# Optimization experiments

Measured on AMD Instinct MI355X. Metric: run time of the kernel, lower is better.

## Reference

```python
import jax, jax.numpy as jnp
import numpy as np

B, S, D, H = 4096, 200, 64, 36
BN_EPS = 1e-5
DICE_EPS = 1e-3


def setup_inputs() -> dict:
    key = jax.random.key(0)
    ks = jax.random.split(key, 6)
    return {
        "history": jax.random.normal(ks[0], (B, S, D), dtype=jnp.float32),
        "candidate": jax.random.normal(ks[1], (B, D), dtype=jnp.float32),
        "W1": jax.random.normal(ks[2], (4 * D, H), dtype=jnp.float32) * 0.05,
        "b1": jax.random.normal(ks[3], (H,), dtype=jnp.float32) * 0.05,
        "gamma": jnp.ones((H,), dtype=jnp.float32),
        "beta": jnp.zeros((H,), dtype=jnp.float32),
        "alpha": jax.random.normal(ks[4], (1,), dtype=jnp.float32),
        "W2": jax.random.normal(ks[5], (H, 1), dtype=jnp.float32) * 0.05,
        "b2": jnp.zeros((1,), dtype=jnp.float32),
    }


def reference(history, candidate, W1, b1, gamma, beta, alpha, W2, b2):
    b, s, d = history.shape
    cand = jnp.broadcast_to(candidate[:, None, :], (b, s, d))
    att_in = jnp.concatenate([cand, history, cand - history, cand * history], axis=-1)
    x = att_in.reshape(b * s, 4 * d)
    # Linear
    h = x @ W1 + b1
    # BatchNorm1d (training mode: batch statistics, biased variance)
    mu = h.mean(axis=0)
    var = h.var(axis=0)
    h = (h - mu) * jax.lax.rsqrt(var + BN_EPS) * gamma + beta
    # Dice: per-row normalization over features, eps=1e-3
    avg = h.mean(axis=1, keepdims=True)
    v = jnp.sum((h - avg) ** 2, axis=1, keepdims=True) / h.shape[1]
    ps = jax.nn.sigmoid((h - avg) / jnp.sqrt(v + DICE_EPS))
    h = ps * h + (1.0 - ps) * alpha * h
    # Output linear -> attention weight per (b, s)
    w = (h @ W2 + b2).reshape(b, s)
    # Weighted sum pooling over sequence
    return jnp.einsum("bs,bsd->bd", w, history)
```

## Files before the change

### kernel.cpp

```cpp
#include <hip/hip_runtime.h>
#include <hip/hip_bf16.h>
#include <math.h>

#define BB 4096
#define SS 200
#define DD 64
#define HH 36
#define NP 48
#define NTI 13
#define NROWSF (4096.0f * 200.0f)
#define PSTRIDE 80

typedef short bf16x8 __attribute__((ext_vector_type(8)));
typedef float f32x4 __attribute__((ext_vector_type(4)));

__device__ __forceinline__ unsigned short f2bf(float f) {
    union { float f; unsigned u; } v; v.f = f;
    unsigned r = v.u + 0x7FFFu + ((v.u >> 16) & 1u);
    return (unsigned short)(r >> 16);
}
__device__ __forceinline__ unsigned f2bf2(float a, float b) {
    union { __hip_bfloat162 h; unsigned u; } v;
    v.h = __float22bfloat162_rn(float2{a, b});
    return v.u;
}

__device__ __forceinline__ void gl_lds16(const void* g, void* l) {
    __builtin_amdgcn_global_load_lds(
        (const __attribute__((address_space(1))) unsigned*)g,
        (__attribute__((address_space(3))) unsigned*)l, 16, 0, 0);
}


__global__ __launch_bounds__(256) void k_wb(const float* __restrict__ cand,
                                            const float* __restrict__ W1,
                                            const float* __restrict__ b1,
                                            unsigned short* __restrict__ WbG,
                                            float* __restrict__ baseG) {
    int b = blockIdx.x, t = threadIdx.x;
    __shared__ float shC[DD];
    if (t < DD) shC[t] = cand[b * DD + t];
    __syncthreads();
    unsigned short* wb = WbG + (size_t)b * (NP * DD);
#pragma unroll
    for (int u = 0; u < 12; ++u) {
        int e = t + u * 256;
        int n = e >> 6, k = e & 63;
        float val = 0.f;
        if (n < HH)
            val = W1[(DD + k) * HH + n] - W1[(2 * DD + k) * HH + n] +
                  shC[k] * W1[(3 * DD + k) * HH + n];
        wb[e] = f2bf(val);
    }
    if (t < NP) {
        float v = 0.f;
        if (t < HH) {
            v = b1[t];
            for (int k = 0; k < DD; ++k)
                v += shC[k] * (W1[k * HH + t] + W1[(2 * DD + k) * HH + t]);
        }
        baseG[b * NP + t] = v;
    }
}

template <bool WB>
__device__ __forceinline__ void prologue512(int b, int t,
                                            const float* __restrict__ hist,
                                            const float* __restrict__ cand,
                                            const float* __restrict__ W1,
                                            const float* __restrict__ b1,
                                            const unsigned short* __restrict__ WbG,
                                            const float* __restrict__ baseG,
                                            float* shHf, unsigned short* shWbT,
                                            float* shC, float* shBase,
                                            float (*shBaseP)[NP]) {
    const float* hsrc = hist + (size_t)b * SS * DD;
    if (WB) {
        const char* hb = (const char*)hsrc;
        char* lb = (char*)shHf;
#pragma unroll
        for (int j = 0; j < 6; ++j) {
            int idx = j * 512 + t;
            int m = idx >> 4, sl = idx & 15;
            gl_lds16(hb + (m << 8) + ((sl ^ (m & 15)) << 4), lb + idx * 16);
        }
        if (t < 128) {
            int idx = 3072 + t;
            int m = idx >> 4, sl = idx & 15;
            gl_lds16(hb + (m << 8) + ((sl ^ (m & 15)) << 4), lb + idx * 16);
        }
        const char* wbsrc = (const char*)(WbG + (size_t)b * (NP * DD));
        if (t < 384) gl_lds16(wbsrc + t * 16, (char*)shWbT + t * 16);
        if (t < NP) shBase[t] = baseG[b * NP + t];
        if (t < 128)
            *(float4*)&shHf[SS * DD + t * 4] = float4{0.f, 0.f, 0.f, 0.f};
        __syncthreads();
    } else {
        if (t < DD) shC[t] = cand[b * DD + t];
        const float4* src = (const float4*)hsrc;
        float4 v[7];
#pragma unroll
        for (int u = 0; u < 6; ++u) v[u] = src[t + u * 512];
        if (t < 128) v[6] = src[t + 3072];
        if (t < 128)
            *(float4*)&shHf[SS * DD + t * 4] = float4{0.f, 0.f, 0.f, 0.f};
        __syncthreads();
#pragma unroll
        for (int u = 0; u < 6; ++u) {
            int G = t + u * 512;
            int sw = (G & ~15) | ((G & 15) ^ ((G >> 4) & 15));
            *(float4*)&shHf[sw * 4] = v[u];
        }
        if (t < 128) {
            int G = t + 3072;
            int sw = (G & ~15) | ((G & 15) ^ ((G >> 4) & 15));
            *(float4*)&shHf[sw * 4] = v[6];
        }
        for (int e = t; e < NP * DD; e += 512) {
            int n = e >> 6, k = e & 63;
            float val = 0.f;
            if (n < HH)
                val = W1[(DD + k) * HH + n] - W1[(2 * DD + k) * HH + n] +
                      shC[k] * W1[(3 * DD + k) * HH + n];
            shWbT[n * DD + k] = f2bf(val);
        }
        if (t < 4 * NP) {
            int g = t / NP, j = t - g * NP;
            float p = 0.f;
            if (j < HH) {
#pragma unroll 4
                for (int k = 16 * g; k < 16 * g + 16; ++k)
                    p += shC[k] * (W1[k * HH + j] + W1[(2 * DD + k) * HH + j]);
            }
            shBaseP[g][j] = p;
        }
        __syncthreads();
        if (t < NP) {
            float val = (t < HH) ? b1[t] : 0.f;
            shBase[t] = val + shBaseP[0][t] + shBaseP[1][t] + shBaseP[2][t] +
                        shBaseP[3][t];
        }
        __syncthreads();
    }
}

__device__ __forceinline__ void load_bfrags(const unsigned short* shWbT, int lane,
                                            bf16x8 (&bfr)[3][2]) {
    int col = lane & 15, q = lane >> 4;
#pragma unroll
    for (int nt = 0; nt < 3; ++nt)
#pragma unroll
        for (int kt = 0; kt < 2; ++kt)
            bfr[nt][kt] = *(const bf16x8*)&shWbT[(nt * 16 + col) * DD + kt * 32 + q * 8];
}

__device__ __forceinline__ bf16x8 load_afrag(const float* shHf, int m, int kt, int q) {
    int s0 = kt * 8 + q * 2;
    int x = m & 15;
    f32x4 x0 = *(const f32x4*)(shHf + m * DD + ((s0 ^ x) << 2));
    f32x4 x1 = *(const f32x4*)(shHf + m * DD + (((s0 + 1) ^ x) << 2));
    union { bf16x8 b8; unsigned u[4]; } a;
    a.u[0] = f2bf2(x0[0], x0[1]);
    a.u[1] = f2bf2(x0[2], x0[3]);
    a.u[2] = f2bf2(x1[0], x1[1]);
    a.u[3] = f2bf2(x1[2], x1[3]);
    return a.b8;
}

__device__ __forceinline__ void gemm_tile(const float* shHf,
                                          const bf16x8 (&bfr)[3][2], int mt, int lane,
                                          f32x4 (&d)[3]) {
    int m = mt * 16 + (lane & 15), q = lane >> 4;
    d[0] = f32x4{0.f, 0.f, 0.f, 0.f};
    d[1] = f32x4{0.f, 0.f, 0.f, 0.f};
    d[2] = f32x4{0.f, 0.f, 0.f, 0.f};
#pragma unroll
    for (int kt = 0; kt < 2; ++kt) {
        bf16x8 a = load_afrag(shHf, m, kt, q);
#pragma unroll
        for (int nt = 0; nt < 3; ++nt)
            d[nt] = __builtin_amdgcn_mfma_f32_16x16x32_bf16(a, bfr[nt][kt], d[nt], 0, 0, 0);
    }
}

template <bool WB, bool RED>
__global__ __launch_bounds__(512, 4) void k_pass1(const float* __restrict__ hist,
                                                  const float* __restrict__ cand,
                                                  const float* __restrict__ W1,
                                                  const float* __restrict__ b1,
                                                  const unsigned short* __restrict__ WbG,
                                                  const float* __restrict__ baseG,
                                                  float* __restrict__ pstat,
                                                  float* __restrict__ gsum,
                                                  float* __restrict__ gsum2) {
    __shared__ __align__(16) float shHf[(SS + 8) * DD];
    __shared__ __align__(16) unsigned short shWbT[NP * DD];
    __shared__ float shC[WB ? 1 : DD], shBase[NP];
    __shared__ float shBaseP[WB ? 1 : 4][NP];
    __shared__ float shP1[8][NP], shP2[8][NP];
    int b = blockIdx.x;
    int t = threadIdx.x, wave = t >> 6, lane = t & 63;
    int col = lane & 15, q = lane >> 4;

    prologue512<WB>(b, t, hist, cand, W1, b1, WbG, baseG, shHf, shWbT, shC,
                    shBase, shBaseP);

    bf16x8 bfr[3][2];
    load_bfrags(shWbT, lane, bfr);
    float basev[3];
#pragma unroll
    for (int nt = 0; nt < 3; ++nt) basev[nt] = shBase[nt * 16 + col];

    float cs1[3] = {0.f, 0.f, 0.f}, cs2[3] = {0.f, 0.f, 0.f};
    for (int mt = wave; mt < NTI; mt += 8) {
        f32x4 d[3];
        gemm_tile(shHf, bfr, mt, lane, d);
        if (mt == 12) {
            int grow0 = 192 + q * 4;
#pragma unroll
            for (int nt = 0; nt < 3; ++nt)
#pragma unroll
                for (int r = 0; r < 4; ++r)
                    if (grow0 + r < SS) {
                        float vv = d[nt][r] + basev[nt];
                        cs1[nt] += vv;
                        cs2[nt] += vv * vv;
                    }
        } else {
#pragma unroll
            for (int nt = 0; nt < 3; ++nt)
#pragma unroll
                for (int r = 0; r < 4; ++r) {
                    float vv = d[nt][r] + basev[nt];
                    cs1[nt] += vv;
                    cs2[nt] += vv * vv;
                }
        }
    }
#pragma unroll
    for (int nt = 0; nt < 3; ++nt) {
        cs1[nt] += __shfl_xor(cs1[nt], 16);
        cs1[nt] += __shfl_xor(cs1[nt], 32);
        cs2[nt] += __shfl_xor(cs2[nt], 16);
        cs2[nt] += __shfl_xor(cs2[nt], 32);
    }
    if (lane < 16) {
#pragma unroll
        for (int nt = 0; nt < 3; ++nt) {
            shP1[wave][nt * 16 + lane] = cs1[nt];
            shP2[wave][nt * 16 + lane] = cs2[nt];
        }
    }
    __syncthreads();
    if (RED) {
        if (t < HH) {
            float s = 0.f;
#pragma unroll
            for (int w = 0; w < 8; ++w) s += shP1[w][t];
            pstat[(size_t)b * PSTRIDE + t] = s;
        } else if (t < 2 * HH) {
            int f = t - HH;
            float s = 0.f;
#pragma unroll
            for (int w = 0; w < 8; ++w) s += shP2[w][f];
            pstat[(size_t)b * PSTRIDE + t] = s;
        }
    } else {
        if (t < HH) {
            float s1 = 0.f, s2 = 0.f;
#pragma unroll
            for (int w = 0; w < 8; ++w) { s1 += shP1[w][t]; s2 += shP2[w][t]; }
            atomicAdd(gsum + t, s1);
            atomicAdd(gsum2 + t, s2);
        }
    }
}

__global__ __launch_bounds__(256) void k_stats_red(const float* __restrict__ pstat,
                                                   const float* __restrict__ gamma,
                                                   const float* __restrict__ beta,
                                                   float* __restrict__ A,
                                                   float* __restrict__ Bc) {
    int f = blockIdx.x, t = threadIdx.x;
    if (f >= HH) {
        if (t == 0) { A[f] = 0.f; Bc[f] = 0.f; }
        return;
    }
    float s1 = 0.f, s2 = 0.f;
    for (int r = t; r < BB; r += 256) {
        s1 += pstat[(size_t)r * PSTRIDE + f];
        s2 += pstat[(size_t)r * PSTRIDE + HH + f];
    }
#pragma unroll
    for (int off = 1; off < 64; off <<= 1) {
        s1 += __shfl_xor(s1, off);
        s2 += __shfl_xor(s2, off);
    }
    __shared__ float a1[4], a2[4];
    if ((t & 63) == 0) { a1[t >> 6] = s1; a2[t >> 6] = s2; }
    __syncthreads();
    if (t == 0) {
        s1 = a1[0] + a1[1] + a1[2] + a1[3];
        s2 = a2[0] + a2[1] + a2[2] + a2[3];
        float mu = s1 * (1.0f / NROWSF);
        float var = s2 * (1.0f / NROWSF) - mu * mu;
        float a = rsqrtf(var + 1e-5f) * gamma[f];
        A[f] = a;
        Bc[f] = beta[f] - mu * a;
    }
}

__global__ void k_stats(const float* __restrict__ gsum, const float* __restrict__ gsum2,
                        const float* __restrict__ gamma, const float* __restrict__ beta,
                        float* __restrict__ A, float* __restrict__ Bc) {
    int t = threadIdx.x;
    if (t < NP) {
        if (t < HH) {
            float mu = gsum[t] * (1.0f / NROWSF);
            float var = gsum2[t] * (1.0f / NROWSF) - mu * mu;
            float a = rsqrtf(var + 1e-5f) * gamma[t];
            A[t] = a;
            Bc[t] = beta[t] - mu * a;
        } else {
            A[t] = 0.f;
            Bc[t] = 0.f;
        }
    }
}

template <bool WB>
__global__ __launch_bounds__(512, 4) void k_pass2(const float* __restrict__ hist,
                                                  const float* __restrict__ cand,
                                                  const float* __restrict__ W1,
                                                  const float* __restrict__ b1,
                                                  const unsigned short* __restrict__ WbG,
                                                  const float* __restrict__ baseG,
                                                  const float* __restrict__ Acoef,
                                                  const float* __restrict__ Bcoef,
                                                  const float* __restrict__ alpha,
                                                  const float* __restrict__ W2,
                                                  const float* __restrict__ b2,
                                                  float* __restrict__ out) {
    __shared__ __align__(16) float shHf[(SS + 8) * DD];
    __shared__ __align__(16) unsigned short shWbT[NP * DD];
    __shared__ float shC[WB ? 1 : DD], shBase[NP];
    __shared__ float shBaseP[WB ? 1 : 4][NP];
    __shared__ float shW[(SS + 8)];
    __shared__ float shPool[8][DD];
    int b = blockIdx.x;
    int t = threadIdx.x, wave = t >> 6, lane = t & 63;
    int col = lane & 15, q = lane >> 4;

    prologue512<WB>(b, t, hist, cand, W1, b1, WbG, baseG, shHf, shWbT, shC,
                    shBase, shBaseP);

    bf16x8 bfr[3][2];
    load_bfrags(shWbT, lane, bfr);
    float baseAB[3], Ar[3], W2r[3];
#pragma unroll
    for (int nt = 0; nt < 3; ++nt) {
        int c = nt * 16 + col;
        Ar[nt] = Acoef[c];
        baseAB[nt] = fmaf(shBase[c], Ar[nt], Bcoef[c]);
        W2r[nt] = (c < HH) ? W2[c] : 0.f;
    }
    float alv = alpha[0], one_m_alv = 1.0f - alv, b2v = b2[0];

    for (int mt = wave; mt < NTI; mt += 8) {
        f32x4 d[3];
        gemm_tile(shHf, bfr, mt, lane, d);
        float hp[3][4];
#pragma unroll
        for (int nt = 0; nt < 3; ++nt)
#pragma unroll
            for (int r = 0; r < 4; ++r)
                hp[nt][r] = fmaf(d[nt][r], Ar[nt], baseAB[nt]);
        float s1[4], s2[4], wsum[4];
#pragma unroll
        for (int r = 0; r < 4; ++r) {
            s1[r] = hp[0][r] + hp[1][r] + hp[2][r];
            s2[r] = hp[0][r] * hp[0][r] + hp[1][r] * hp[1][r] + hp[2][r] * hp[2][r];
            s1[r] += __shfl_xor(s1[r], 1);
            s1[r] += __shfl_xor(s1[r], 2);
            s1[r] += __shfl_xor(s1[r], 4);
            s1[r] += __shfl_xor(s1[r], 8);
            s2[r] += __shfl_xor(s2[r], 1);
            s2[r] += __shfl_xor(s2[r], 2);
            s2[r] += __shfl_xor(s2[r], 4);
            s2[r] += __shfl_xor(s2[r], 8);
        }
#pragma unroll
        for (int r = 0; r < 4; ++r) {
            float avg = s1[r] * (1.0f / (float)HH);
            float var = s2[r] * (1.0f / (float)HH) - avg * avg;
            float inv = rsqrtf(var + 1e-3f);
            float wv = 0.f;
#pragma unroll
            for (int nt = 0; nt < 3; ++nt) {
                float z = (hp[nt][r] - avg) * inv;
                float ps = 1.0f / (1.0f + __expf(-z));
                float f = fmaf(ps, one_m_alv, alv);
                wv = fmaf(hp[nt][r] * f, W2r[nt], wv);
            }
            wsum[r] = wv;
            wsum[r] += __shfl_xor(wsum[r], 1);
            wsum[r] += __shfl_xor(wsum[r], 2);
            wsum[r] += __shfl_xor(wsum[r], 4);
            wsum[r] += __shfl_xor(wsum[r], 8);
        }
        if (col == 0) {
            float4 o = {wsum[0] + b2v, wsum[1] + b2v, wsum[2] + b2v, wsum[3] + b2v};
            *(float4*)&shW[mt * 16 + q * 4] = o;
        }
    }
    __syncthreads();
    {
        float p = 0.f;
        for (int s = wave; s < SS; s += 8) {
            int sw = (((lane >> 2) ^ (s & 15)) << 2) | (lane & 3);
            p = fmaf(shW[s], shHf[s * DD + sw], p);
        }
        shPool[wave][lane] = p;
    }
    __syncthreads();
    if (t < DD) {
        float s = 0.f;
#pragma unroll
        for (int w = 0; w < 8; ++w) s += shPool[w][t];
        out[b * DD + t] = s;
    }
}

extern "C" void kernel_launch(void* const* d_in, const int* in_sizes, int n_in,
                              void* d_out, int out_size, void* d_ws, size_t ws_size,
                              hipStream_t stream) {
    const float* hist = (const float*)d_in[0];
    const float* cand = (const float*)d_in[1];
    const float* W1 = (const float*)d_in[2];
    const float* b1 = (const float*)d_in[3];
    const float* gamma = (const float*)d_in[4];
    const float* beta = (const float*)d_in[5];
    const float* alpha = (const float*)d_in[6];
    const float* W2 = (const float*)d_in[7];
    const float* b2 = (const float*)d_in[8];
    float* out = (float*)d_out;
    float* ws = (float*)d_ws;

    const size_t pstatF = (size_t)BB * PSTRIDE;
    const size_t baseF = (size_t)BB * NP;
    const size_t wbBytes = (size_t)BB * NP * DD * 2;
    const size_t fullNeed = (pstatF + 2 * NP + baseF) * 4 + wbBytes;
    const size_t midNeed = (pstatF + 2 * NP) * 4;

    if (ws_size >= fullNeed) {
        float* pstat = ws;
        float* A = pstat + pstatF;
        float* Bc = A + NP;
        float* baseG = Bc + NP;
        unsigned short* WbG = (unsigned short*)(baseG + baseF);
        k_wb<<<BB, 256, 0, stream>>>(cand, W1, b1, WbG, baseG);
        k_pass1<true, true><<<BB, 512, 0, stream>>>(hist, cand, W1, b1, WbG, baseG,
                                                    pstat, nullptr, nullptr);
        k_stats_red<<<NP, 256, 0, stream>>>(pstat, gamma, beta, A, Bc);
        k_pass2<true><<<BB, 512, 0, stream>>>(hist, cand, W1, b1, WbG, baseG, A, Bc,
                                              alpha, W2, b2, out);
    } else if (ws_size >= midNeed) {
        float* pstat = ws;
        float* A = pstat + pstatF;
        float* Bc = A + NP;
        k_pass1<false, true><<<BB, 512, 0, stream>>>(hist, cand, W1, b1, nullptr,
                                                     nullptr, pstat, nullptr, nullptr);
        k_stats_red<<<NP, 256, 0, stream>>>(pstat, gamma, beta, A, Bc);
        k_pass2<false><<<BB, 512, 0, stream>>>(hist, cand, W1, b1, nullptr, nullptr,
                                               A, Bc, alpha, W2, b2, out);
    } else {
        float* gsum = ws;
        float* gsum2 = ws + NP;
        float* A = ws + 2 * NP;
        float* Bc = ws + 3 * NP;
        hipMemsetAsync(gsum, 0, 2 * NP * sizeof(float), stream);
        k_pass1<false, false><<<BB, 512, 0, stream>>>(hist, cand, W1, b1, nullptr,
                                                      nullptr, nullptr, gsum, gsum2);
        k_stats<<<1, 64, 0, stream>>>(gsum, gsum2, gamma, beta, A, Bc);
        k_pass2<false><<<BB, 512, 0, stream>>>(hist, cand, W1, b1, nullptr, nullptr,
                                               A, Bc, alpha, W2, b2, out);
    }
}
```

Baseline: 419.1 us.

## Make pass kernels process eight batches per block with register prefetch

In the full-workspace path, each block of pass1 and pass2 now processes eight consecutive batch rows instead of one. The next row's history tile, folded weights and base vector are prefetched into registers while the current row computes, then committed to shared memory. This is meant to hide global load latency and amortise block launch and setup. In exchange, the grid shrinks to 512 blocks, which lowers the number of resident waves per CU. It also replaces the async global-to-LDS copies and raises register pressure.

```diff
diff --git a/kernel.cpp b/kernel.cpp
--- a/kernel.cpp
+++ b/kernel.cpp
@@ -10,6 +10,8 @@
 #define NTI 13
 #define NROWSF (4096.0f * 200.0f)
 #define PSTRIDE 80
+#define BPB 8
+#define NBLK (BB / BPB)
 
 typedef short bf16x8 __attribute__((ext_vector_type(8)));
 typedef float f32x4 __attribute__((ext_vector_type(4)));
@@ -63,85 +65,36 @@
     }
 }
 
-template <bool WB>
-__device__ __forceinline__ void prologue512(int b, int t,
+__device__ __forceinline__ void issue_loads(int b, int t,
                                             const float* __restrict__ hist,
-                                            const float* __restrict__ cand,
-                                            const float* __restrict__ W1,
-                                            const float* __restrict__ b1,
                                             const unsigned short* __restrict__ WbG,
                                             const float* __restrict__ baseG,
-                                            float* shHf, unsigned short* shWbT,
-                                            float* shC, float* shBase,
-                                            float (*shBaseP)[NP]) {
-    const float* hsrc = hist + (size_t)b * SS * DD;
-    if (WB) {
-        const char* hb = (const char*)hsrc;
-        char* lb = (char*)shHf;
-#pragma unroll
-        for (int j = 0; j < 6; ++j) {
-            int idx = j * 512 + t;
-            int m = idx >> 4, sl = idx & 15;
-            gl_lds16(hb + (m << 8) + ((sl ^ (m & 15)) << 4), lb + idx * 16);
-        }
-        if (t < 128) {
-            int idx = 3072 + t;
-            int m = idx >> 4, sl = idx & 15;
-            gl_lds16(hb + (m << 8) + ((sl ^ (m & 15)) << 4), lb + idx * 16);
-        }
-        const char* wbsrc = (const char*)(WbG + (size_t)b * (NP * DD));
-        if (t < 384) gl_lds16(wbsrc + t * 16, (char*)shWbT + t * 16);
-        if (t < NP) shBase[t] = baseG[b * NP + t];
-        if (t < 128)
-            *(float4*)&shHf[SS * DD + t * 4] = float4{0.f, 0.f, 0.f, 0.f};
-        __syncthreads();
-    } else {
-        if (t < DD) shC[t] = cand[b * DD + t];
-        const float4* src = (const float4*)hsrc;
-        float4 v[7];
-#pragma unroll
-        for (int u = 0; u < 6; ++u) v[u] = src[t + u * 512];
-        if (t < 128) v[6] = src[t + 3072];
-        if (t < 128)
-            *(float4*)&shHf[SS * DD + t * 4] = float4{0.f, 0.f, 0.f, 0.f};
-        __syncthreads();
-#pragma unroll
-        for (int u = 0; u < 6; ++u) {
-            int G = t + u * 512;
-            int sw = (G & ~15) | ((G & 15) ^ ((G >> 4) & 15));
-            *(float4*)&shHf[sw * 4] = v[u];
-        }
-        if (t < 128) {
-            int G = t + 3072;
-            int sw = (G & ~15) | ((G & 15) ^ ((G >> 4) & 15));
-            *(float4*)&shHf[sw * 4] = v[6];
-        }
-        for (int e = t; e < NP * DD; e += 512) {
-            int n = e >> 6, k = e & 63;
-            float val = 0.f;
-            if (n < HH)
-                val = W1[(DD + k) * HH + n] - W1[(2 * DD + k) * HH + n] +
-                      shC[k] * W1[(3 * DD + k) * HH + n];
-            shWbT[n * DD + k] = f2bf(val);
-        }
-        if (t < 4 * NP) {
-            int g = t / NP, j = t - g * NP;
-            float p = 0.f;
-            if (j < HH) {
-#pragma unroll 4
-                for (int k = 16 * g; k < 16 * g + 16; ++k)
-                    p += shC[k] * (W1[k * HH + j] + W1[(2 * DD + k) * HH + j]);
-            }
-            shBaseP[g][j] = p;
-        }
-        __syncthreads();
-        if (t < NP) {
-            float val = (t < HH) ? b1[t] : 0.f;
-            shBase[t] = val + shBaseP[0][t] + shBaseP[1][t] + shBaseP[2][t] +
-                        shBaseP[3][t];
-        }
-        __syncthreads();
-    }
+                                            float4 (&v)[7], uint4& w, float& bse) {
+    const float4* src = (const float4*)(hist + (size_t)b * SS * DD);
+#pragma unroll
+    for (int u = 0; u < 6; ++u) v[u] = src[t + u * 512];
+    if (t < 128) v[6] = src[t + 3072];
+    const uint4* wsrc = (const uint4*)(WbG + (size_t)b * (NP * DD));
+    if (t < 384) w = wsrc[t];
+    if (t < NP) bse = baseG[b * NP + t];
+}
+
+__device__ __forceinline__ void commit(int t, const float4 (&v)[7], const uint4& w,
+                                       float bse, float* shHf,
+                                       unsigned short* shWbT, float* shBase) {
+#pragma unroll
+    for (int u = 0; u < 6; ++u) {
+        int G = t + u * 512;
+        int sw = (G & ~15) | ((G & 15) ^ ((G >> 4) & 15));
+        *(float4*)&shHf[sw * 4] = v[u];
+    }
+    if (t < 128) {
+        int G = t + 3072;
+        int sw = (G & ~15) | ((G & 15) ^ ((G >> 4) & 15));
+        *(float4*)&shHf[sw * 4] = v[6];
+    }
+    if (t < 384) *(uint4*)((char*)shWbT + t * 16) = w;
+    if (t < NP) shBase[t] = bse;
 }
 
 __device__ __forceinline__ void load_bfrags(const unsigned short* shWbT, int lane,
@@ -183,95 +136,215 @@
     }
 }
 
-template <bool WB, bool RED>
-__global__ __launch_bounds__(512, 4) void k_pass1(const float* __restrict__ hist,
-                                                  const float* __restrict__ cand,
-                                                  const float* __restrict__ W1,
-                                                  const float* __restrict__ b1,
-                                                  const unsigned short* __restrict__ WbG,
-                                                  const float* __restrict__ baseG,
-                                                  float* __restrict__ pstat,
-                                                  float* __restrict__ gsum,
-                                                  float* __restrict__ gsum2) {
+__global__ __launch_bounds__(512, 4) void k_pass1m(const float* __restrict__ hist,
+                                                   const unsigned short* __restrict__ WbG,
+                                                   const float* __restrict__ baseG,
+                                                   float* __restrict__ pstat) {
     __shared__ __align__(16) float shHf[(SS + 8) * DD];
     __shared__ __align__(16) unsigned short shWbT[NP * DD];
-    __shared__ float shC[WB ? 1 : DD], shBase[NP];
-    __shared__ float shBaseP[WB ? 1 : 4][NP];
+    __shared__ float shBase[NP];
     __shared__ float shP1[8][NP], shP2[8][NP];
-    int b = blockIdx.x;
     int t = threadIdx.x, wave = t >> 6, lane = t & 63;
     int col = lane & 15, q = lane >> 4;
-
-    prologue512<WB>(b, t, hist, cand, W1, b1, WbG, baseG, shHf, shWbT, shC,
-                    shBase, shBaseP);
-
-    bf16x8 bfr[3][2];
-    load_bfrags(shWbT, lane, bfr);
-    float basev[3];
-#pragma unroll
-    for (int nt = 0; nt < 3; ++nt) basev[nt] = shBase[nt * 16 + col];
-
-    float cs1[3] = {0.f, 0.f, 0.f}, cs2[3] = {0.f, 0.f, 0.f};
-    for (int mt = wave; mt < NTI; mt += 8) {
-        f32x4 d[3];
-        gemm_tile(shHf, bfr, mt, lane, d);
-        if (mt == 12) {
-            int grow0 = 192 + q * 4;
-#pragma unroll
-            for (int nt = 0; nt < 3; ++nt)
-#pragma unroll
-                for (int r = 0; r < 4; ++r)
-                    if (grow0 + r < SS) {
+    int b0 = blockIdx.x * BPB;
+
+    if (t < 128)
+        *(float4*)&shHf[SS * DD + t * 4] = float4{0.f, 0.f, 0.f, 0.f};
+    {
+        float4 v[7]; uint4 w; float bse = 0.f;
+        issue_loads(b0, t, hist, WbG, baseG, v, w, bse);
+        commit(t, v, w, bse, shHf, shWbT, shBase);
+    }
+    __syncthreads();
+
+    for (int i = 0; i < BPB; ++i) {
+        int b = b0 + i;
+        float4 nv[7]; uint4 nw; float nbse = 0.f;
+        if (i + 1 < BPB)
+            issue_loads(b0 + i + 1, t, hist, WbG, baseG, nv, nw, nbse);
+
+        bf16x8 bfr[3][2];
+        load_bfrags(shWbT, lane, bfr);
+        float basev[3];
+#pragma unroll
+        for (int nt = 0; nt < 3; ++nt) basev[nt] = shBase[nt * 16 + col];
+
+        float cs1[3] = {0.f, 0.f, 0.f}, cs2[3] = {0.f, 0.f, 0.f};
+        for (int mt = wave; mt < NTI; mt += 8) {
+            f32x4 d[3];
+            gemm_tile(shHf, bfr, mt, lane, d);
+            if (mt == 12) {
+                int grow0 = 192 + q * 4;
+#pragma unroll
+                for (int nt = 0; nt < 3; ++nt)
+#pragma unroll
+                    for (int r = 0; r < 4; ++r)
+                        if (grow0 + r < SS) {
+                            float vv = d[nt][r] + basev[nt];
+                            cs1[nt] += vv;
+                            cs2[nt] += vv * vv;
+                        }
+            } else {
+#pragma unroll
+                for (int nt = 0; nt < 3; ++nt)
+#pragma unroll
+                    for (int r = 0; r < 4; ++r) {
                         float vv = d[nt][r] + basev[nt];
                         cs1[nt] += vv;
                         cs2[nt] += vv * vv;
                     }
-        } else {
-#pragma unroll
-            for (int nt = 0; nt < 3; ++nt)
-#pragma unroll
-                for (int r = 0; r < 4; ++r) {
-                    float vv = d[nt][r] + basev[nt];
-                    cs1[nt] += vv;
-                    cs2[nt] += vv * vv;
-                }
-        }
-    }
-#pragma unroll
-    for (int nt = 0; nt < 3; ++nt) {
-        cs1[nt] += __shfl_xor(cs1[nt], 16);
-        cs1[nt] += __shfl_xor(cs1[nt], 32);
-        cs2[nt] += __shfl_xor(cs2[nt], 16);
-        cs2[nt] += __shfl_xor(cs2[nt], 32);
-    }
-    if (lane < 16) {
+            }
+        }
 #pragma unroll
         for (int nt = 0; nt < 3; ++nt) {
-            shP1[wave][nt * 16 + lane] = cs1[nt];
-            shP2[wave][nt * 16 + lane] = cs2[nt];
-        }
-    }
-    __syncthreads();
-    if (RED) {
+            cs1[nt] += __shfl_xor(cs1[nt], 16);
+            cs1[nt] += __shfl_xor(cs1[nt], 32);
+            cs2[nt] += __shfl_xor(cs2[nt], 16);
+            cs2[nt] += __shfl_xor(cs2[nt], 32);
+        }
+        if (lane < 16) {
+#pragma unroll
+            for (int nt = 0; nt < 3; ++nt) {
+                shP1[wave][nt * 16 + lane] = cs1[nt];
+                shP2[wave][nt * 16 + lane] = cs2[nt];
+            }
+        }
+        __syncthreads();
         if (t < HH) {
             float s = 0.f;
 #pragma unroll
-            for (int w = 0; w < 8; ++w) s += shP1[w][t];
+            for (int w8 = 0; w8 < 8; ++w8) s += shP1[w8][t];
             pstat[(size_t)b * PSTRIDE + t] = s;
         } else if (t < 2 * HH) {
             int f = t - HH;
             float s = 0.f;
 #pragma unroll
-            for (int w = 0; w < 8; ++w) s += shP2[w][f];
+            for (int w8 = 0; w8 < 8; ++w8) s += shP2[w8][f];
             pstat[(size_t)b * PSTRIDE + t] = s;
         }
-    } else {
-        if (t < HH) {
-            float s1 = 0.f, s2 = 0.f;
-#pragma unroll
-            for (int w = 0; w < 8; ++w) { s1 += shP1[w][t]; s2 += shP2[w][t]; }
-            atomicAdd(gsum + t, s1);
-            atomicAdd(gsum2 + t, s2);
+        if (i + 1 < BPB) {
+            commit(t, nv, nw, nbse, shHf, shWbT, shBase);
+            __syncthreads();
+        }
+    }
+}
+
+__global__ __launch_bounds__(512, 4) void k_pass2m(const float* __restrict__ hist,
+                                                   const unsigned short* __restrict__ WbG,
+                                                   const float* __restrict__ baseG,
+                                                   const float* __restrict__ Acoef,
+                                                   const float* __restrict__ Bcoef,
+                                                   const float* __restrict__ alpha,
+                                                   const float* __restrict__ W2,
+                                                   const float* __restrict__ b2,
+                                                   float* __restrict__ out) {
+    __shared__ __align__(16) float shHf[(SS + 8) * DD];
+    __shared__ __align__(16) unsigned short shWbT[NP * DD];
+    __shared__ float shBase[NP];
+    __shared__ float shW[(SS + 8)];
+    __shared__ float shPool[8][DD];
+    int t = threadIdx.x, wave = t >> 6, lane = t & 63;
+    int col = lane & 15, q = lane >> 4;
+    int b0 = blockIdx.x * BPB;
+
+    float Ar[3], Bcr[3], W2r[3];
+#pragma unroll
+    for (int nt = 0; nt < 3; ++nt) {
+        int c = nt * 16 + col;
+        Ar[nt] = Acoef[c];
+        Bcr[nt] = Bcoef[c];
+        W2r[nt] = (c < HH) ? W2[c] : 0.f;
+    }
+    float alv = alpha[0], one_m_alv = 1.0f - alv, b2v = b2[0];
+
+    if (t < 128)
+        *(float4*)&shHf[SS * DD + t * 4] = float4{0.f, 0.f, 0.f, 0.f};
+    {
+        float4 v[7]; uint4 w; float bse = 0.f;
+        issue_loads(b0, t, hist, WbG, baseG, v, w, bse);
+        commit(t, v, w, bse, shHf, shWbT, shBase);
+    }
+    __syncthreads();
+
+    for (int i = 0; i < BPB; ++i) {
+        int b = b0 + i;
+        float4 nv[7]; uint4 nw; float nbse = 0.f;
+        if (i + 1 < BPB)
+            issue_loads(b0 + i + 1, t, hist, WbG, baseG, nv, nw, nbse);
+
+        bf16x8 bfr[3][2];
+        load_bfrags(shWbT, lane, bfr);
+        float baseAB[3];
+#pragma unroll
+        for (int nt = 0; nt < 3; ++nt)
+            baseAB[nt] = fmaf(shBase[nt * 16 + col], Ar[nt], Bcr[nt]);
+
+        for (int mt = wave; mt < NTI; mt += 8) {
+            f32x4 d[3];
+            gemm_tile(shHf, bfr, mt, lane, d);
+            float hp[3][4];
+#pragma unroll
+            for (int nt = 0; nt < 3; ++nt)
+#pragma unroll
+                for (int r = 0; r < 4; ++r)
+                    hp[nt][r] = fmaf(d[nt][r], Ar[nt], baseAB[nt]);
+            float s1[4], s2[4], wsum[4];
+#pragma unroll
+            for (int r = 0; r < 4; ++r) {
+                s1[r] = hp[0][r] + hp[1][r] + hp[2][r];
+                s2[r] = hp[0][r] * hp[0][r] + hp[1][r] * hp[1][r] + hp[2][r] * hp[2][r];
+                s1[r] += __shfl_xor(s1[r], 1);
+                s1[r] += __shfl_xor(s1[r], 2);
+                s1[r] += __shfl_xor(s1[r], 4);
+                s1[r] += __shfl_xor(s1[r], 8);
+                s2[r] += __shfl_xor(s2[r], 1);
+                s2[r] += __shfl_xor(s2[r], 2);
+                s2[r] += __shfl_xor(s2[r], 4);
+                s2[r] += __shfl_xor(s2[r], 8);
+            }
+#pragma unroll
+            for (int r = 0; r < 4; ++r) {
+                float avg = s1[r] * (1.0f / (float)HH);
+                float var = s2[r] * (1.0f / (float)HH) - avg * avg;
+                float inv = rsqrtf(var + 1e-3f);
+                float wv = 0.f;
+#pragma unroll
+                for (int nt = 0; nt < 3; ++nt) {
+                    float z = (hp[nt][r] - avg) * inv;
+                    float ps = 1.0f / (1.0f + __expf(-z));
+                    float f = fmaf(ps, one_m_alv, alv);
+                    wv = fmaf(hp[nt][r] * f, W2r[nt], wv);
+                }
+                wsum[r] = wv;
+                wsum[r] += __shfl_xor(wsum[r], 1);
+                wsum[r] += __shfl_xor(wsum[r], 2);
+                wsum[r] += __shfl_xor(wsum[r], 4);
+                wsum[r] += __shfl_xor(wsum[r], 8);
+            }
+            if (col == 0) {
+                float4 o = {wsum[0] + b2v, wsum[1] + b2v, wsum[2] + b2v, wsum[3] + b2v};
+                *(float4*)&shW[mt * 16 + q * 4] = o;
+            }
+        }
+        __syncthreads();
+        {
+            float p = 0.f;
+            for (int s = wave; s < SS; s += 8) {
+                int sw = (((lane >> 2) ^ (s & 15)) << 2) | (lane & 3);
+                p = fmaf(shW[s], shHf[s * DD + sw], p);
+            }
+            shPool[wave][lane] = p;
+        }
+        __syncthreads();
+        if (t < DD) {
+            float s = 0.f;
+#pragma unroll
+            for (int w8 = 0; w8 < 8; ++w8) s += shPool[w8][t];
+            out[b * DD + t] = s;
+        }
+        if (i + 1 < BPB) {
+            commit(t, nv, nw, nbse, shHf, shWbT, shBase);
+            __syncthreads();
         }
     }
 }
@@ -328,31 +401,172 @@
     }
 }
 
-template <bool WB>
-__global__ __launch_bounds__(512, 4) void k_pass2(const float* __restrict__ hist,
-                                                  const float* __restrict__ cand,
-                                                  const float* __restrict__ W1,
-                                                  const float* __restrict__ b1,
-                                                  const unsigned short* __restrict__ WbG,
-                                                  const float* __restrict__ baseG,
-                                                  const float* __restrict__ Acoef,
-                                                  const float* __restrict__ Bcoef,
-                                                  const float* __restrict__ alpha,
-                                                  const float* __restrict__ W2,
-                                                  const float* __restrict__ b2,
-                                                  float* __restrict__ out) {
+__device__ __forceinline__ void prologue_fb(int b, int t,
+                                            const float* __restrict__ hist,
+                                            const float* __restrict__ cand,
+                                            const float* __restrict__ W1,
+                                            const float* __restrict__ b1,
+                                            float* shHf, unsigned short* shWbT,
+                                            float* shC, float* shBase,
+                                            float (*shBaseP)[NP]) {
+    if (t < DD) shC[t] = cand[b * DD + t];
+    const float4* src = (const float4*)(hist + (size_t)b * SS * DD);
+    float4 v[7];
+#pragma unroll
+    for (int u = 0; u < 6; ++u) v[u] = src[t + u * 512];
+    if (t < 128) v[6] = src[t + 3072];
+    if (t < 128)
+        *(float4*)&shHf[SS * DD + t * 4] = float4{0.f, 0.f, 0.f, 0.f};
+    __syncthreads();
+#pragma unroll
+    for (int u = 0; u < 6; ++u) {
+        int G = t + u * 512;
+        int sw = (G & ~15) | ((G & 15) ^ ((G >> 4) & 15));
+        *(float4*)&shHf[sw * 4] = v[u];
+    }
+    if (t < 128) {
+        int G = t + 3072;
+        int sw = (G & ~15) | ((G & 15) ^ ((G >> 4) & 15));
+        *(float4*)&shHf[sw * 4] = v[6];
+    }
+    for (int e = t; e < NP * DD; e += 512) {
+        int n = e >> 6, k = e & 63;
+        float val = 0.f;
+        if (n < HH)
+            val = W1[(DD + k) * HH + n] - W1[(2 * DD + k) * HH + n] +
+                  shC[k] * W1[(3 * DD + k) * HH + n];
+        shWbT[n * DD + k] = f2bf(val);
+    }
+    if (t < 4 * NP) {
+        int g = t / NP, j = t - g * NP;
+        float p = 0.f;
+        if (j < HH) {
+#pragma unroll 4
+            for (int k = 16 * g; k < 16 * g + 16; ++k)
+                p += shC[k] * (W1[k * HH + j] + W1[(2 * DD + k) * HH + j]);
+        }
+        shBaseP[g][j] = p;
+    }
+    __syncthreads();
+    if (t < NP) {
+        float val = (t < HH) ? b1[t] : 0.f;
+        shBase[t] = val + shBaseP[0][t] + shBaseP[1][t] + shBaseP[2][t] +
+                    shBaseP[3][t];
+    }
+    __syncthreads();
+}
+
+template <bool RED>
+__global__ __launch_bounds__(512, 4) void k_pass1f(const float* __restrict__ hist,
+                                                   const float* __restrict__ cand,
+                                                   const float* __restrict__ W1,
+                                                   const float* __restrict__ b1,
+                                                   float* __restrict__ pstat,
+                                                   float* __restrict__ gsum,
+                                                   float* __restrict__ gsum2) {
     __shared__ __align__(16) float shHf[(SS + 8) * DD];
     __shared__ __align__(16) unsigned short shWbT[NP * DD];
-    __shared__ float shC[WB ? 1 : DD], shBase[NP];
-    __shared__ float shBaseP[WB ? 1 : 4][NP];
+    __shared__ float shC[DD], shBase[NP];
+    __shared__ float shBaseP[4][NP];
+    __shared__ float shP1[8][NP], shP2[8][NP];
+    int b = blockIdx.x;
+    int t = threadIdx.x, wave = t >> 6, lane = t & 63;
+    int col = lane & 15, q = lane >> 4;
+
+    prologue_fb(b, t, hist, cand, W1, b1, shHf, shWbT, shC, shBase, shBaseP);
+
+    bf16x8 bfr[3][2];
+    load_bfrags(shWbT, lane, bfr);
+    float basev[3];
+#pragma unroll
+    for (int nt = 0; nt < 3; ++nt) basev[nt] = shBase[nt * 16 + col];
+
+    float cs1[3] = {0.f, 0.f, 0.f}, cs2[3] = {0.f, 0.f, 0.f};
+    for (int mt = wave; mt < NTI; mt += 8) {
+        f32x4 d[3];
+        gemm_tile(shHf, bfr, mt, lane, d);
+        if (mt == 12) {
+            int grow0 = 192 + q * 4;
+#pragma unroll
+            for (int nt = 0; nt < 3; ++nt)
+#pragma unroll
+                for (int r = 0; r < 4; ++r)
+                    if (grow0 + r < SS) {
+                        float vv = d[nt][r] + basev[nt];
+                        cs1[nt] += vv;
+                        cs2[nt] += vv * vv;
+                    }
+        } else {
+#pragma unroll
+            for (int nt = 0; nt < 3; ++nt)
+#pragma unroll
+                for (int r = 0; r < 4; ++r) {
+                    float vv = d[nt][r] + basev[nt];
+                    cs1[nt] += vv;
+                    cs2[nt] += vv * vv;
+                }
+        }
+    }
+#pragma unroll
+    for (int nt = 0; nt < 3; ++nt) {
+        cs1[nt] += __shfl_xor(cs1[nt], 16);
+        cs1[nt] += __shfl_xor(cs1[nt], 32);
+        cs2[nt] += __shfl_xor(cs2[nt], 16);
+        cs2[nt] += __shfl_xor(cs2[nt], 32);
+    }
+    if (lane < 16) {
+#pragma unroll
+        for (int nt = 0; nt < 3; ++nt) {
+            shP1[wave][nt * 16 + lane] = cs1[nt];
+            shP2[wave][nt * 16 + lane] = cs2[nt];
+        }
+    }
+    __syncthreads();
+    if (RED) {
+        if (t < HH) {
+            float s = 0.f;
+#pragma unroll
+            for (int w = 0; w < 8; ++w) s += shP1[w][t];
+            pstat[(size_t)b * PSTRIDE + t] = s;
+        } else if (t < 2 * HH) {
+            int f = t - HH;
+            float s = 0.f;
+#pragma unroll
+            for (int w = 0; w < 8; ++w) s += shP2[w][f];
+            pstat[(size_t)b * PSTRIDE + t] = s;
+        }
+    } else {
+        if (t < HH) {
+            float s1 = 0.f, s2 = 0.f;
+#pragma unroll
+            for (int w = 0; w < 8; ++w) { s1 += shP1[w][t]; s2 += shP2[w][t]; }
+            atomicAdd(gsum + t, s1);
+            atomicAdd(gsum2 + t, s2);
+        }
+    }
+}
+
+__global__ __launch_bounds__(512, 4) void k_pass2f(const float* __restrict__ hist,
+                                                   const float* __restrict__ cand,
+                                                   const float* __restrict__ W1,
+                                                   const float* __restrict__ b1,
+                                                   const float* __restrict__ Acoef,
+                                                   const float* __restrict__ Bcoef,
+                                                   const float* __restrict__ alpha,
+                                                   const float* __restrict__ W2,
+                                                   const float* __restrict__ b2,
+                                                   float* __restrict__ out) {
+    __shared__ __align__(16) float shHf[(SS + 8) * DD];
+    __shared__ __align__(16) unsigned short shWbT[NP * DD];
+    __shared__ float shC[DD], shBase[NP];
+    __shared__ float shBaseP[4][NP];
     __shared__ float shW[(SS + 8)];
     __shared__ float shPool[8][DD];
     int b = blockIdx.x;
     int t = threadIdx.x, wave = t >> 6, lane = t & 63;
     int col = lane & 15, q = lane >> 4;
 
-    prologue512<WB>(b, t, hist, cand, W1, b1, WbG, baseG, shHf, shWbT, shC,
-                    shBase, shBaseP);
+    prologue_fb(b, t, hist, cand, W1, b1, shHf, shWbT, shC, shBase, shBaseP);
 
     bf16x8 bfr[3][2];
     load_bfrags(shWbT, lane, bfr);
@@ -459,30 +673,29 @@
         float* baseG = Bc + NP;
         unsigned short* WbG = (unsigned short*)(baseG + baseF);
         k_wb<<<BB, 256, 0, stream>>>(cand, W1, b1, WbG, baseG);
-        k_pass1<true, true><<<BB, 512, 0, stream>>>(hist, cand, W1, b1, WbG, baseG,
-                                                    pstat, nullptr, nullptr);
+        k_pass1m<<<NBLK, 512, 0, stream>>>(hist, WbG, baseG, pstat);
         k_stats_red<<<NP, 256, 0, stream>>>(pstat, gamma, beta, A, Bc);
-        k_pass2<true><<<BB, 512, 0, stream>>>(hist, cand, W1, b1, WbG, baseG, A, Bc,
-                                              alpha, W2, b2, out);
+        k_pass2m<<<NBLK, 512, 0, stream>>>(hist, WbG, baseG, A, Bc, alpha, W2, b2,
+                                           out);
     } else if (ws_size >= midNeed) {
         float* pstat = ws;
         float* A = pstat + pstatF;
         float* Bc = A + NP;
-        k_pass1<false, true><<<BB, 512, 0, stream>>>(hist, cand, W1, b1, nullptr,
-                                                     nullptr, pstat, nullptr, nullptr);
+        k_pass1f<true><<<BB, 512, 0, stream>>>(hist, cand, W1, b1, pstat, nullptr,
+                                               nullptr);
         k_stats_red<<<NP, 256, 0, stream>>>(pstat, gamma, beta, A, Bc);
-        k_pass2<false><<<BB, 512, 0, stream>>>(hist, cand, W1, b1, nullptr, nullptr,
-                                               A, Bc, alpha, W2, b2, out);
+        k_pass2f<<<BB, 512, 0, stream>>>(hist, cand, W1, b1, A, Bc, alpha, W2, b2,
+                                         out);
     } else {
         float* gsum = ws;
         float* gsum2 = ws + NP;
         float* A = ws + 2 * NP;
         float* Bc = ws + 3 * NP;
         hipMemsetAsync(gsum, 0, 2 * NP * sizeof(float), stream);
-        k_pass1<false, false><<<BB, 512, 0, stream>>>(hist, cand, W1, b1, nullptr,
-                                                      nullptr, nullptr, gsum, gsum2);
+        k_pass1f<false><<<BB, 512, 0, stream>>>(hist, cand, W1, b1, nullptr, gsum,
+                                                gsum2);
         k_stats<<<1, 64, 0, stream>>>(gsum, gsum2, gamma, beta, A, Bc);
-        k_pass2<false><<<BB, 512, 0, stream>>>(hist, cand, W1, b1, nullptr, nullptr,
-                                               A, Bc, alpha, W2, b2, out);
-    }
-}
+        k_pass2f<<<BB, 512, 0, stream>>>(hist, cand, W1, b1, A, Bc, alpha, W2, b2,
+                                         out);
+    }
+}
```

Measured after the change: 513.1 us. 22.4% more time.
